# Kernel tuning notes

Hardware: AMD Instinct MI355X
Metric: run time of the kernel (lower is better)

The kernel has to match this reference:

```python
import jax, jax.numpy as jnp
import numpy as np

N = 50000      # nodes
E = 800000     # edges (avg degree 16)
F0 = 3         # node feature dim
EF = 3         # edge feature dim
C = 4          # num classes


def _lin_params(k, din, dout):
    k1, k2 = jax.random.split(k)
    s = 1.0 / np.sqrt(din)
    W = jax.random.uniform(k1, (dout, din), jnp.float32, -s, s)
    b = jax.random.uniform(k2, (dout,), jnp.float32, -s, s)
    return W, b


def setup_inputs() -> dict:
    key = jax.random.key(0)
    ks = jax.random.split(key, 8)
    x = jax.random.normal(ks[0], (N, F0), jnp.float32)
    edge_index = jax.random.randint(ks[1], (2, E), 0, N, jnp.int32)
    edge_attr = jax.random.uniform(ks[2], (E, EF), dtype=jnp.float32)
    W1, b1 = _lin_params(ks[3], 2 * F0 + EF, 128)
    W2, b2 = _lin_params(ks[4], 2 * 128 + EF, 64)
    W3, b3 = _lin_params(ks[5], 2 * 64 + EF, 32)
    Wc, bc = _lin_params(ks[6], 32, C)
    return dict(x=x, edge_index=edge_index, edge_attr=edge_attr,
                W1=W1, b1=b1, W2=W2, b2=b2, W3=W3, b3=b3, Wc=Wc, bc=bc)


def _edgeconv(x, src, dst, ea, W, b, n):
    # message = Linear(cat([x_i, x_j, edge_attr])); aggregated by scatter-add to dst (x_i side).
    # Split W so the node-side matmuls happen once per node instead of per edge.
    f = x.shape[1]
    Wi, Wj, We = W[:, :f], W[:, f:2 * f], W[:, 2 * f:]
    ai = x @ Wi.T   # [N, out]
    aj = x @ Wj.T   # [N, out]
    msg = ai[dst] + aj[src] + ea @ We.T + b  # [E_aug, out]
    return jax.ops.segment_sum(msg, dst, num_segments=n)


def reference(x, edge_index, edge_attr, W1, b1, W2, b2, W3, b3, Wc, bc):
    n = x.shape[0]
    loops = jnp.arange(n, dtype=edge_index.dtype)
    src = jnp.concatenate([edge_index[0], loops])  # x_j indices
    dst = jnp.concatenate([edge_index[1], loops])  # x_i indices (aggregation targets)
    ea = jnp.concatenate([edge_attr, jnp.zeros((n, edge_attr.shape[1]), edge_attr.dtype)])
    h = jax.nn.relu(_edgeconv(x, src, dst, ea, W1, b1, n))
    h = jax.nn.relu(_edgeconv(h, src, dst, ea, W2, b2, n))
    h = _edgeconv(h, src, dst, ea, W3, b3, n)  # no relu after conv3 in the original
    logits = h @ Wc.T + bc
    return jax.nn.log_softmax(logits, axis=1)
```

## Files before the change

### kernel.cpp

```cpp
#include <hip/hip_runtime.h>
#include <math.h>


static inline size_t align256(size_t x) { return (x + 255) & ~size_t(255); }

typedef unsigned short ushort_t;
using frag8  = __attribute__((ext_vector_type(8))) short;
using f32x4v = __attribute__((ext_vector_type(4))) float;
using half8  = __attribute__((ext_vector_type(8))) _Float16;

__device__ inline unsigned short f2bf(float f) {
    unsigned u = __float_as_uint(f);
    unsigned r = (u + 0x7fffu + ((u >> 16) & 1u)) >> 16;
    return (unsigned short)r;
}
__device__ inline float bflo(unsigned u) { return __uint_as_float(u << 16); }
__device__ inline float bfhi(unsigned u) { return __uint_as_float(u & 0xffff0000u); }


__global__ __launch_bounds__(256) void build_count(
    const int* __restrict__ ei, int* __restrict__ count,
    int* __restrict__ pos, int E)
{
    int e4 = (blockIdx.x * 256 + threadIdx.x) * 4;
    if (e4 >= E) return;
    if (e4 + 3 < E) {
        int4 d = *(const int4*)(ei + E + e4);
        int4 po;
        po.x = atomicAdd(&count[d.x], 1);
        po.y = atomicAdd(&count[d.y], 1);
        po.z = atomicAdd(&count[d.z], 1);
        po.w = atomicAdd(&count[d.w], 1);
        *(int4*)(pos + e4) = po;
    } else {
        for (int e = e4; e < E; ++e)
            pos[e] = atomicAdd(&count[ei[E + e]], 1);
    }
}

__global__ __launch_bounds__(256) void scan_pass1(
    const int* __restrict__ count, int* __restrict__ rowstart,
    int* __restrict__ bsum, int n)
{
    __shared__ int sh[256];
    const int tid = threadIdx.x;
    const int base = blockIdx.x * 1024 + tid * 4;
    int v0 = 0, v1 = 0, v2 = 0, v3 = 0;
    if (base + 3 < n) {
        int4 c = *(const int4*)(count + base);
        v0 = c.x; v1 = c.y; v2 = c.z; v3 = c.w;
    } else {
        if (base + 0 < n) v0 = count[base + 0];
        if (base + 1 < n) v1 = count[base + 1];
        if (base + 2 < n) v2 = count[base + 2];
        if (base + 3 < n) v3 = count[base + 3];
    }
    int tsum = v0 + v1 + v2 + v3;
    sh[tid] = tsum;
    __syncthreads();
    for (int off = 1; off < 256; off <<= 1) {
        int t = (tid >= off) ? sh[tid - off] : 0;
        __syncthreads();
        sh[tid] += t;
        __syncthreads();
    }
    int excl = sh[tid] - tsum;
    int p0 = excl + v0, p1 = p0 + v1, p2 = p1 + v2, p3 = p2 + v3;
    if (base + 0 < n) rowstart[base + 1] = p0;
    if (base + 1 < n) rowstart[base + 2] = p1;
    if (base + 2 < n) rowstart[base + 3] = p2;
    if (base + 3 < n) rowstart[base + 4] = p3;
    if (tid == 255) bsum[blockIdx.x] = sh[255];
}

__global__ __launch_bounds__(64) void scan_pass2(
    const int* __restrict__ bsum, int* __restrict__ bexcl, int nb)
{
    int lane = threadIdx.x;
    int own = (lane < nb) ? bsum[lane] : 0;
    int x = own;
    for (int off = 1; off < 64; off <<= 1) {
        int t = __shfl_up(x, off);
        if (lane >= off) x += t;
    }
    bexcl[lane] = x - own;
}

__global__ __launch_bounds__(256) void scan_pass3(
    int* __restrict__ rowstart, const int* __restrict__ bexcl,
    const float* __restrict__ x, float4* __restrict__ xpad, int n)
{
    int j = blockIdx.x * 256 + threadIdx.x;
    if (j > n) return;
    if (j == 0) {
        rowstart[0] = 0;
    } else {
        int b = (j - 1) >> 10;
        if (b > 0) rowstart[j] += bexcl[b];
    }
    if (j < n)
        xpad[j] = make_float4(x[j * 3], x[j * 3 + 1], x[j * 3 + 2], 0.f);
}

__global__ __launch_bounds__(256) void csr_scatter(
    const int* __restrict__ ei, const float* __restrict__ ea,
    const int* __restrict__ pos, const int* __restrict__ rowstart,
    uint2* __restrict__ csrp, int E)
{
    int e4 = (blockIdx.x * 256 + threadIdx.x) * 4;
    if (e4 >= E) return;
    if (e4 + 3 < E) {
        int4 s = *(const int4*)(ei + e4);
        int4 d = *(const int4*)(ei + E + e4);
        int4 po = *(const int4*)(pos + e4);
        float4 a = *(const float4*)(ea + (size_t)e4 * 3);
        float4 b = *(const float4*)(ea + (size_t)e4 * 3 + 4);
        float4 c = *(const float4*)(ea + (size_t)e4 * 3 + 8);
        float ev[12] = { a.x, a.y, a.z, a.w, b.x, b.y, b.z, b.w, c.x, c.y, c.z, c.w };
        int sv[4] = { s.x, s.y, s.z, s.w };
        int dv[4] = { d.x, d.y, d.z, d.w };
        int pv[4] = { po.x, po.y, po.z, po.w };
        #pragma unroll
        for (int r = 0; r < 4; ++r) {
            uint2 p;
            p.x = (unsigned)f2bf(ev[r * 3 + 0]) | ((unsigned)f2bf(ev[r * 3 + 1]) << 16);
            p.y = (unsigned)f2bf(ev[r * 3 + 2]) | ((unsigned)sv[r] << 16);
            csrp[rowstart[dv[r]] + pv[r]] = p;
        }
    } else {
        for (int e = e4; e < E; ++e) {
            uint2 p;
            p.x = (unsigned)f2bf(ea[e * 3 + 0]) | ((unsigned)f2bf(ea[e * 3 + 1]) << 16);
            p.y = (unsigned)f2bf(ea[e * 3 + 2]) | ((unsigned)ei[e] << 16);
            csrp[rowstart[ei[E + e]] + pos[e]] = p;
        }
    }
}


__global__ __launch_bounds__(256) void prep_collapse(
    const float* __restrict__ W3, const float* __restrict__ b3,
    const float* __restrict__ Wc, const float* __restrict__ bc,
    float* __restrict__ AB, float* __restrict__ consts)
{
    int t = threadIdx.x;
    for (int idx = t; idx < 512; idx += 256) {
        int j = idx >> 6, k = idx & 63;
        int jj = j & 3;
        int base = (j >= 4) ? 64 : 0;
        float s = 0.f;
        #pragma unroll
        for (int c = 0; c < 32; ++c)
            s += Wc[jj * 32 + c] * W3[c * 131 + base + k];
        AB[idx] = s;
    }
    if (t < 4) {
        float db = 0.f;
        for (int c = 0; c < 32; ++c) db += Wc[t * 32 + c] * b3[c];
        consts[t] = db;
        consts[4 + t] = bc[t];
        for (int q = 0; q < 3; ++q) {
            float s = 0.f;
            for (int c = 0; c < 32; ++c) s += Wc[t * 32 + c] * W3[c * 131 + 128 + q];
            consts[8 + t * 3 + q] = s;
        }
    }
}


__global__ __launch_bounds__(256) void h1_fused(
    const float4* __restrict__ xpad, const float* __restrict__ W1,
    const float* __restrict__ b1, const int* __restrict__ rowstart,
    const uint2* __restrict__ csrp, float4* __restrict__ eagg4,
    ushort_t* __restrict__ h1, int n_nodes)
{
    __shared__ float sM[10 * 128];
    const int tid = threadIdx.x;
    for (int t = tid; t < 1280; t += 256) {
        int k = t >> 7, c = t & 127;
        sM[t] = (k < 9) ? W1[c * 9 + k] : b1[c];
    }
    __syncthreads();

    int wl = tid & 63;
    int grp = wl >> 3, ch8 = wl & 7;
    int n = blockIdx.x * 32 + (tid >> 6) * 8 + grp;
    if (n >= n_nodes) return;

    int s0 = rowstart[n], s1 = rowstart[n + 1];
    float xx = 0.f, xy = 0.f, xz = 0.f, ex = 0.f, ey = 0.f, ez = 0.f;
    for (int i = s0 + ch8; i < s1; i += 8) {
        uint2 p = csrp[i];
        int s = (int)(p.y >> 16);
        ex += bflo(p.x); ey += bfhi(p.x); ez += bflo(p.y);
        float4 xv = xpad[s];
        xx += xv.x; xy += xv.y; xz += xv.z;
    }
    #pragma unroll
    for (int off = 1; off < 8; off <<= 1) {
        xx += __shfl_xor(xx, off); xy += __shfl_xor(xy, off); xz += __shfl_xor(xz, off);
        ex += __shfl_xor(ex, off); ey += __shfl_xor(ey, off); ez += __shfl_xor(ez, off);
    }

    float deg = (float)(s1 - s0 + 1);
    float4 xs = xpad[n];
    float v[10] = { deg * xs.x, deg * xs.y, deg * xs.z,
                    xs.x + xx, xs.y + xy, xs.z + xz,
                    ex, ey, ez, deg };
    int cb = ch8 * 16;
    #pragma unroll
    for (int g = 0; g < 2; ++g) {
        float hv[8];
        #pragma unroll
        for (int q = 0; q < 8; ++q) {
            int c = cb + g * 8 + q;
            float h = 0.f;
            #pragma unroll
            for (int k = 0; k < 10; ++k) h += v[k] * sM[k * 128 + c];
            hv[q] = fmaxf(h, 0.f);
        }
        uint4 u;
        u.x = (unsigned)f2bf(hv[0]) | ((unsigned)f2bf(hv[1]) << 16);
        u.y = (unsigned)f2bf(hv[2]) | ((unsigned)f2bf(hv[3]) << 16);
        u.z = (unsigned)f2bf(hv[4]) | ((unsigned)f2bf(hv[5]) << 16);
        u.w = (unsigned)f2bf(hv[6]) | ((unsigned)f2bf(hv[7]) << 16);
        *(uint4*)(h1 + (size_t)n * 128 + cb + g * 8) = u;
    }
    if (ch8 == 0) eagg4[n] = make_float4(ex, ey, ez, 0.f);
}


__global__ __launch_bounds__(256) void gemm_mfma(
    const ushort_t* __restrict__ h1, const float* __restrict__ W2,
    float* __restrict__ AI2, _Float16* __restrict__ AJ2, int n_nodes)
{
    constexpr int KP = 136;
    __shared__ ushort_t sB[128 * KP];

    const int tid = threadIdx.x;
    for (int t = tid; t < 128 * 128; t += 256) {
        int jg = t >> 7, k = t & 127;
        float w = (jg < 64) ? W2[jg * 259 + k] : W2[(jg - 64) * 259 + 128 + k];
        sB[jg * KP + k] = f2bf(w);
    }
    __syncthreads();

    const int wave = tid >> 6, lane = tid & 63;
    const int m = lane & 15, quad = lane >> 4;
    const int mwave = blockIdx.x * 64 + wave * 16;

    int arow = mwave + m;
    int arow_c = arow < n_nodes ? arow : (n_nodes - 1);

    frag8 a[4];
    #pragma unroll
    for (int ks = 0; ks < 4; ++ks)
        a[ks] = *(const frag8*)(h1 + (size_t)arow_c * 128 + ks * 32 + quad * 8);

    f32x4v acc[8];
    #pragma unroll
    for (int t = 0; t < 8; ++t) acc[t] = (f32x4v)(0.f);

    #pragma unroll
    for (int t = 0; t < 8; ++t) {
        #pragma unroll
        for (int ks = 0; ks < 4; ++ks) {
            frag8 b = *(const frag8*)(sB + (t * 16 + m) * KP + ks * 32 + quad * 8);
            acc[t] = __builtin_amdgcn_mfma_f32_16x16x32_bf16(a[ks], b, acc[t], 0, 0, 0);
        }
    }

    #pragma unroll
    for (int reg = 0; reg < 4; ++reg) {
        int grow = mwave + quad * 4 + reg;
        if (grow >= n_nodes) continue;
        #pragma unroll
        for (int t = 0; t < 4; ++t)
            AI2[(size_t)grow * 64 + t * 16 + m] = acc[t][reg];
        #pragma unroll
        for (int t = 4; t < 8; ++t)
            AJ2[(size_t)grow * 64 + (t - 4) * 16 + m] = (_Float16)acc[t][reg];
    }
}


__global__ __launch_bounds__(256) void gather2(
    const float* __restrict__ AI2, const _Float16* __restrict__ AJ2,
    const float* __restrict__ W2, const float* __restrict__ b2,
    const float4* __restrict__ eagg4, const int* __restrict__ rowstart,
    const uint2* __restrict__ csrp, const float* __restrict__ AB,
    float* __restrict__ U, float* __restrict__ Z, int n_nodes)
{
    __shared__ float sAB[512];
    __shared__ float sWe[192];
    const int tid = threadIdx.x;
    for (int t = tid; t < 512; t += 256) sAB[t] = AB[t];
    for (int t = tid; t < 192; t += 256) {
        int c = t / 3, q = t % 3;
        sWe[t] = W2[c * 259 + 256 + q];
    }
    __syncthreads();

    int wl = tid & 63;
    int grp = wl >> 3, ch8 = wl & 7;
    int n = blockIdx.x * 32 + (tid >> 6) * 8 + grp;
    if (n >= n_nodes) return;

    int s0 = rowstart[n], s1 = rowstart[n + 1];

    half8 hacc = (half8)(_Float16)0.f;
    for (int base = s0; base < s1; base += 8) {
        int j = base + ch8;
        if (j >= s1) j = s1 - 1;
        int myidx = (int)(csrp[j].y >> 16);
        int cnt = s1 - base; if (cnt > 8) cnt = 8;
        #pragma unroll
        for (int k = 0; k < 8; ++k) {
            int s = __shfl(myidx, grp * 8 + k);
            if (k < cnt) {
                half8 v = *(const half8*)(AJ2 + (size_t)s * 64 + ch8 * 8);
                hacc += v;
            }
        }
    }
    float acc[8];
    #pragma unroll
    for (int q = 0; q < 8; ++q) acc[q] = (float)hacc[q];

    float deg = (float)(s1 - s0 + 1);
    float4 e4 = eagg4[n];
    const float* aip = AI2 + (size_t)n * 64 + ch8 * 8;
    float4 aiA = *(const float4*)(aip);
    float4 aiB = *(const float4*)(aip + 4);
    half8 su = *(const half8*)(AJ2 + (size_t)n * 64 + ch8 * 8);
    float4 bA = *(const float4*)(b2 + ch8 * 8);
    float4 bB = *(const float4*)(b2 + ch8 * 8 + 4);
    float av[8] = { aiA.x, aiA.y, aiA.z, aiA.w, aiB.x, aiB.y, aiB.z, aiB.w };
    float bv[8] = { bA.x, bA.y, bA.z, bA.w, bB.x, bB.y, bB.z, bB.w };
    float r[8];
    #pragma unroll
    for (int q = 0; q < 8; ++q) {
        int c = ch8 * 8 + q;
        float we = sWe[c * 3] * e4.x + sWe[c * 3 + 1] * e4.y + sWe[c * 3 + 2] * e4.z;
        r[q] = fmaxf(deg * (av[q] + bv[q]) + (float)su[q] + we + acc[q], 0.f);
    }
    float pj[8];
    #pragma unroll
    for (int j = 0; j < 8; ++j) {
        float4 wA = *(const float4*)(sAB + j * 64 + ch8 * 8);
        float4 wB = *(const float4*)(sAB + j * 64 + ch8 * 8 + 4);
        pj[j] = r[0] * wA.x + r[1] * wA.y + r[2] * wA.z + r[3] * wA.w
              + r[4] * wB.x + r[5] * wB.y + r[6] * wB.z + r[7] * wB.w;
    }
    #pragma unroll
    for (int off = 1; off < 8; off <<= 1)
        #pragma unroll
        for (int j = 0; j < 8; ++j) pj[j] += __shfl_xor(pj[j], off);

    if (ch8 == 0) {
        *(float4*)(U + (size_t)n * 4) = make_float4(pj[0], pj[1], pj[2], pj[3]);
        *(float4*)(Z + (size_t)n * 4) = make_float4(pj[4], pj[5], pj[6], pj[7]);
    }
}


__global__ __launch_bounds__(256) void final_softmax(
    const float* __restrict__ U, const float* __restrict__ Z,
    const float4* __restrict__ eagg4, const int* __restrict__ rowstart,
    const uint2* __restrict__ csrp, const float* __restrict__ consts,
    float* __restrict__ out, int n_nodes)
{
    int wl = threadIdx.x & 63;
    int grp = wl >> 3, ch8 = wl & 7;
    int n = blockIdx.x * 32 + (threadIdx.x >> 6) * 8 + grp;
    if (n >= n_nodes) return;

    int s0 = rowstart[n], s1 = rowstart[n + 1];
    float ax = 0.f, ay = 0.f, az = 0.f, aw = 0.f;
    for (int i = s0 + ch8; i < s1; i += 8) {
        int s = (int)(csrp[i].y >> 16);
        float4 z = *(const float4*)(Z + (size_t)s * 4);
        ax += z.x; ay += z.y; az += z.z; aw += z.w;
    }
    #pragma unroll
    for (int off = 1; off < 8; off <<= 1) {
        ax += __shfl_xor(ax, off); ay += __shfl_xor(ay, off);
        az += __shfl_xor(az, off); aw += __shfl_xor(aw, off);
    }
    if (ch8 != 0) return;

    float deg = (float)(s1 - s0 + 1);
    float4 u = *(const float4*)(U + (size_t)n * 4);
    float4 zs = *(const float4*)(Z + (size_t)n * 4);
    float4 e4 = eagg4[n];
    float av[4] = { ax + zs.x, ay + zs.y, az + zs.z, aw + zs.w };
    float uv[4] = { u.x, u.y, u.z, u.w };
    float lg[4];
    #pragma unroll
    for (int j = 0; j < 4; ++j) {
        lg[j] = deg * (uv[j] + consts[j]) + av[j] + consts[4 + j]
              + consts[8 + j * 3] * e4.x + consts[9 + j * 3] * e4.y
              + consts[10 + j * 3] * e4.z;
    }
    float m = fmaxf(fmaxf(lg[0], lg[1]), fmaxf(lg[2], lg[3]));
    float lse = logf(expf(lg[0] - m) + expf(lg[1] - m) + expf(lg[2] - m) + expf(lg[3] - m));
    *(float4*)(out + (size_t)n * 4) =
        make_float4(lg[0] - m - lse, lg[1] - m - lse, lg[2] - m - lse, lg[3] - m - lse);
}


extern "C" void kernel_launch(void* const* d_in, const int* in_sizes, int n_in,
                              void* d_out, int out_size, void* d_ws, size_t ws_size,
                              hipStream_t stream)
{
    const float* x    = (const float*)d_in[0];
    const int*   ei   = (const int*)  d_in[1];
    const float* ea   = (const float*)d_in[2];
    const float* W1   = (const float*)d_in[3];
    const float* b1   = (const float*)d_in[4];
    const float* W2   = (const float*)d_in[5];
    const float* b2   = (const float*)d_in[6];
    const float* W3   = (const float*)d_in[7];
    const float* b3   = (const float*)d_in[8];
    const float* Wc   = (const float*)d_in[9];
    const float* bc   = (const float*)d_in[10];
    float* out = (float*)d_out;

    const int N = in_sizes[0] / 3;
    const int E = in_sizes[1] / 2;

    char* ws = (char*)d_ws;
    size_t off = 0;
    int*    count    = (int*)(ws + off);            off = align256(off + (size_t)N * 4);
    int*    pos      = (int*)(ws + off);            off = align256(off + (size_t)E * 4);
    int*    rowstart = (int*)(ws + off);            off = align256(off + (size_t)(N + 1) * 4);
    uint2*  csrp     = (uint2*)(ws + off);          off = align256(off + (size_t)E * 8);
    int*    bsum     = (int*)(ws + off);            off = align256(off + 256);
    int*    bexcl    = (int*)(ws + off);            off = align256(off + 256);
    float*  AB       = (float*)(ws + off);          off = align256(off + 512 * 4);
    float*  consts   = (float*)(ws + off);          off = align256(off + 32 * 4);
    float4* xpad     = (float4*)(ws + off);         off = align256(off + (size_t)N * 16);
    float4* eagg4    = (float4*)(ws + off);         off = align256(off + (size_t)N * 16);
    ushort_t* h1buf  = (ushort_t*)(ws + off);       off = align256(off + (size_t)N * 128 * 2);
    float*  AI2      = (float*)(ws + off);          off = align256(off + (size_t)N * 64 * 4);
    _Float16* AJ2    = (_Float16*)(ws + off);       off = align256(off + (size_t)N * 64 * 2);
    float*  Ubuf     = (float*)(ws + off);          off = align256(off + (size_t)N * 16);
    float*  Zbuf     = (float*)(ws + off);          off = align256(off + (size_t)N * 16);
    (void)ws_size;

    hipMemsetAsync(count, 0, (size_t)N * 4, stream);

    const int eb4 = ((E + 3) / 4 + 255) / 256;
    build_count<<<eb4, 256, 0, stream>>>(ei, count, pos, E);

    const int nb1 = (N + 1023) / 1024;
    scan_pass1<<<nb1, 256, 0, stream>>>(count, rowstart, bsum, N);
    scan_pass2<<<1, 64, 0, stream>>>(bsum, bexcl, nb1);
    scan_pass3<<<(N + 1 + 255) / 256, 256, 0, stream>>>(rowstart, bexcl, x, xpad, N);
    csr_scatter<<<eb4, 256, 0, stream>>>(ei, ea, pos, rowstart, csrp, E);

    prep_collapse<<<1, 256, 0, stream>>>(W3, b3, Wc, bc, AB, consts);

    const int gb = (N + 31) / 32;

    h1_fused<<<gb, 256, 0, stream>>>(xpad, W1, b1, rowstart, csrp, eagg4, h1buf, N);

    gemm_mfma<<<(N + 63) / 64, 256, 0, stream>>>(h1buf, W2, AI2, AJ2, N);
    gather2<<<gb, 256, 0, stream>>>(AI2, AJ2, W2, b2, eagg4, rowstart, csrp, AB, Ubuf, Zbuf, N);

    final_softmax<<<gb, 256, 0, stream>>>(Ubuf, Zbuf, eagg4, rowstart, csrp, consts, out, N);
}
```

Before: 209.4 us.

## Fuse layer-1 aggregation with MFMA GEMM via shared memory; merge small prep kernels

```diff
diff --git a/kernel.cpp b/kernel.cpp
--- a/kernel.cpp
+++ b/kernel.cpp
@@ -73,17 +73,55 @@
     if (tid == 255) bsum[blockIdx.x] = sh[255];
 }
 
-__global__ __launch_bounds__(64) void scan_pass2(
-    const int* __restrict__ bsum, int* __restrict__ bexcl, int nb)
-{
-    int lane = threadIdx.x;
-    int own = (lane < nb) ? bsum[lane] : 0;
-    int x = own;
-    for (int off = 1; off < 64; off <<= 1) {
-        int t = __shfl_up(x, off);
-        if (lane >= off) x += t;
-    }
-    bexcl[lane] = x - own;
+__global__ __launch_bounds__(256) void mid_fused(
+    const int* __restrict__ bsum, int* __restrict__ bexcl, int nb,
+    const float* __restrict__ W3, const float* __restrict__ b3,
+    const float* __restrict__ Wc, const float* __restrict__ bc,
+    float* __restrict__ AB, float* __restrict__ consts,
+    const float* __restrict__ W2, ushort_t* __restrict__ W2bf)
+{
+    const int t = threadIdx.x;
+    if (blockIdx.x == 0) {
+        if (t < 64) {
+            int own = (t < nb) ? bsum[t] : 0;
+            int x = own;
+            for (int off = 1; off < 64; off <<= 1) {
+                int s = __shfl_up(x, off);
+                if (t >= off) x += s;
+            }
+            bexcl[t] = x - own;
+        }
+    } else if (blockIdx.x == 1) {
+        for (int idx = t; idx < 512; idx += 256) {
+            int j = idx >> 6, k = idx & 63;
+            int jj = j & 3;
+            int base = (j >= 4) ? 64 : 0;
+            float s = 0.f;
+            #pragma unroll
+            for (int c = 0; c < 32; ++c)
+                s += Wc[jj * 32 + c] * W3[c * 131 + base + k];
+            AB[idx] = s;
+        }
+        if (t < 4) {
+            float db = 0.f;
+            for (int c = 0; c < 32; ++c) db += Wc[t * 32 + c] * b3[c];
+            consts[t] = db;
+            consts[4 + t] = bc[t];
+            for (int q = 0; q < 3; ++q) {
+                float s = 0.f;
+                for (int c = 0; c < 32; ++c) s += Wc[t * 32 + c] * W3[c * 131 + 128 + q];
+                consts[8 + t * 3 + q] = s;
+            }
+        }
+    } else {
+        int i0 = (blockIdx.x - 2) * 4096 + t;
+        int i1 = (blockIdx.x - 1) * 4096;
+        for (int idx = i0; idx < i1; idx += 256) {
+            int jg = idx >> 7, k = idx & 127;
+            float w = (jg < 64) ? W2[jg * 259 + k] : W2[(jg - 64) * 259 + 128 + k];
+            W2bf[idx] = f2bf(w);
+        }
+    }
 }
 
 __global__ __launch_bounds__(256) void scan_pass3(
@@ -138,43 +176,17 @@
 }
 
 
-__global__ __launch_bounds__(256) void prep_collapse(
-    const float* __restrict__ W3, const float* __restrict__ b3,
-    const float* __restrict__ Wc, const float* __restrict__ bc,
-    float* __restrict__ AB, float* __restrict__ consts)
-{
-    int t = threadIdx.x;
-    for (int idx = t; idx < 512; idx += 256) {
-        int j = idx >> 6, k = idx & 63;
-        int jj = j & 3;
-        int base = (j >= 4) ? 64 : 0;
-        float s = 0.f;
-        #pragma unroll
-        for (int c = 0; c < 32; ++c)
-            s += Wc[jj * 32 + c] * W3[c * 131 + base + k];
-        AB[idx] = s;
-    }
-    if (t < 4) {
-        float db = 0.f;
-        for (int c = 0; c < 32; ++c) db += Wc[t * 32 + c] * b3[c];
-        consts[t] = db;
-        consts[4 + t] = bc[t];
-        for (int q = 0; q < 3; ++q) {
-            float s = 0.f;
-            for (int c = 0; c < 32; ++c) s += Wc[t * 32 + c] * W3[c * 131 + 128 + q];
-            consts[8 + t * 3 + q] = s;
-        }
-    }
-}
-
-
-__global__ __launch_bounds__(256) void h1_fused(
+__global__ __launch_bounds__(256) void h1_gemm(
     const float4* __restrict__ xpad, const float* __restrict__ W1,
     const float* __restrict__ b1, const int* __restrict__ rowstart,
     const uint2* __restrict__ csrp, float4* __restrict__ eagg4,
-    ushort_t* __restrict__ h1, int n_nodes)
-{
+    const ushort_t* __restrict__ W2bf,
+    float* __restrict__ AI2, _Float16* __restrict__ AJ2, int n_nodes)
+{
+    constexpr int HS = 144;
     __shared__ float sM[10 * 128];
+    __shared__ ushort_t sH[64 * HS];
+
     const int tid = threadIdx.x;
     for (int t = tid; t < 1280; t += 256) {
         int k = t >> 7, c = t & 127;
@@ -182,80 +194,66 @@
     }
     __syncthreads();
 
-    int wl = tid & 63;
-    int grp = wl >> 3, ch8 = wl & 7;
-    int n = blockIdx.x * 32 + (tid >> 6) * 8 + grp;
-    if (n >= n_nodes) return;
-
-    int s0 = rowstart[n], s1 = rowstart[n + 1];
-    float xx = 0.f, xy = 0.f, xz = 0.f, ex = 0.f, ey = 0.f, ez = 0.f;
-    for (int i = s0 + ch8; i < s1; i += 8) {
-        uint2 p = csrp[i];
-        int s = (int)(p.y >> 16);
-        ex += bflo(p.x); ey += bfhi(p.x); ez += bflo(p.y);
-        float4 xv = xpad[s];
-        xx += xv.x; xy += xv.y; xz += xv.z;
-    }
-    #pragma unroll
-    for (int off = 1; off < 8; off <<= 1) {
-        xx += __shfl_xor(xx, off); xy += __shfl_xor(xy, off); xz += __shfl_xor(xz, off);
-        ex += __shfl_xor(ex, off); ey += __shfl_xor(ey, off); ez += __shfl_xor(ez, off);
-    }
-
-    float deg = (float)(s1 - s0 + 1);
-    float4 xs = xpad[n];
-    float v[10] = { deg * xs.x, deg * xs.y, deg * xs.z,
-                    xs.x + xx, xs.y + xy, xs.z + xz,
-                    ex, ey, ez, deg };
-    int cb = ch8 * 16;
-    #pragma unroll
-    for (int g = 0; g < 2; ++g) {
-        float hv[8];
-        #pragma unroll
-        for (int q = 0; q < 8; ++q) {
-            int c = cb + g * 8 + q;
-            float h = 0.f;
+    const int base = blockIdx.x * 64;
+    const int wave = tid >> 6, wl = tid & 63;
+    const int grp = wl >> 3, ch8 = wl & 7;
+
+    #pragma unroll
+    for (int pass = 0; pass < 2; ++pass) {
+        int nl = pass * 32 + wave * 8 + grp;
+        int n = base + nl;
+        float hv[16];
+        if (n < n_nodes) {
+            int s0 = rowstart[n], s1 = rowstart[n + 1];
+            float xx = 0.f, xy = 0.f, xz = 0.f, ex = 0.f, ey = 0.f, ez = 0.f;
+            for (int i = s0 + ch8; i < s1; i += 8) {
+                uint2 p = csrp[i];
+                int s = (int)(p.y >> 16);
+                ex += bflo(p.x); ey += bfhi(p.x); ez += bflo(p.y);
+                float4 xv = xpad[s];
+                xx += xv.x; xy += xv.y; xz += xv.z;
+            }
             #pragma unroll
-            for (int k = 0; k < 10; ++k) h += v[k] * sM[k * 128 + c];
-            hv[q] = fmaxf(h, 0.f);
-        }
-        uint4 u;
-        u.x = (unsigned)f2bf(hv[0]) | ((unsigned)f2bf(hv[1]) << 16);
-        u.y = (unsigned)f2bf(hv[2]) | ((unsigned)f2bf(hv[3]) << 16);
-        u.z = (unsigned)f2bf(hv[4]) | ((unsigned)f2bf(hv[5]) << 16);
-        u.w = (unsigned)f2bf(hv[6]) | ((unsigned)f2bf(hv[7]) << 16);
-        *(uint4*)(h1 + (size_t)n * 128 + cb + g * 8) = u;
-    }
-    if (ch8 == 0) eagg4[n] = make_float4(ex, ey, ez, 0.f);
-}
-
-
-__global__ __launch_bounds__(256) void gemm_mfma(
-    const ushort_t* __restrict__ h1, const float* __restrict__ W2,
-    float* __restrict__ AI2, _Float16* __restrict__ AJ2, int n_nodes)
-{
-    constexpr int KP = 136;
-    __shared__ ushort_t sB[128 * KP];
-
-    const int tid = threadIdx.x;
-    for (int t = tid; t < 128 * 128; t += 256) {
-        int jg = t >> 7, k = t & 127;
-        float w = (jg < 64) ? W2[jg * 259 + k] : W2[(jg - 64) * 259 + 128 + k];
-        sB[jg * KP + k] = f2bf(w);
+            for (int off = 1; off < 8; off <<= 1) {
+                xx += __shfl_xor(xx, off); xy += __shfl_xor(xy, off); xz += __shfl_xor(xz, off);
+                ex += __shfl_xor(ex, off); ey += __shfl_xor(ey, off); ez += __shfl_xor(ez, off);
+            }
+            float deg = (float)(s1 - s0 + 1);
+            float4 xs = xpad[n];
+            float v[10] = { deg * xs.x, deg * xs.y, deg * xs.z,
+                            xs.x + xx, xs.y + xy, xs.z + xz,
+                            ex, ey, ez, deg };
+            #pragma unroll
+            for (int q = 0; q < 16; ++q) {
+                int c = ch8 * 16 + q;
+                float h = 0.f;
+                #pragma unroll
+                for (int k = 0; k < 10; ++k) h += v[k] * sM[k * 128 + c];
+                hv[q] = fmaxf(h, 0.f);
+            }
+            if (ch8 == 0) eagg4[n] = make_float4(ex, ey, ez, 0.f);
+        } else {
+            #pragma unroll
+            for (int q = 0; q < 16; ++q) hv[q] = 0.f;
+        }
+        #pragma unroll
+        for (int g = 0; g < 2; ++g) {
+            uint4 u;
+            u.x = (unsigned)f2bf(hv[g * 8 + 0]) | ((unsigned)f2bf(hv[g * 8 + 1]) << 16);
+            u.y = (unsigned)f2bf(hv[g * 8 + 2]) | ((unsigned)f2bf(hv[g * 8 + 3]) << 16);
+            u.z = (unsigned)f2bf(hv[g * 8 + 4]) | ((unsigned)f2bf(hv[g * 8 + 5]) << 16);
+            u.w = (unsigned)f2bf(hv[g * 8 + 6]) | ((unsigned)f2bf(hv[g * 8 + 7]) << 16);
+            *(uint4*)(sH + nl * HS + ch8 * 16 + g * 8) = u;
+        }
     }
     __syncthreads();
 
-    const int wave = tid >> 6, lane = tid & 63;
-    const int m = lane & 15, quad = lane >> 4;
-    const int mwave = blockIdx.x * 64 + wave * 16;
-
-    int arow = mwave + m;
-    int arow_c = arow < n_nodes ? arow : (n_nodes - 1);
+    const int m = wl & 15, quad = wl >> 4;
 
     frag8 a[4];
     #pragma unroll
     for (int ks = 0; ks < 4; ++ks)
-        a[ks] = *(const frag8*)(h1 + (size_t)arow_c * 128 + ks * 32 + quad * 8);
+        a[ks] = *(const frag8*)(sH + (wave * 16 + m) * HS + ks * 32 + quad * 8);
 
     f32x4v acc[8];
     #pragma unroll
@@ -265,14 +263,14 @@
     for (int t = 0; t < 8; ++t) {
         #pragma unroll
         for (int ks = 0; ks < 4; ++ks) {
-            frag8 b = *(const frag8*)(sB + (t * 16 + m) * KP + ks * 32 + quad * 8);
+            frag8 b = *(const frag8*)(W2bf + (t * 16 + m) * 128 + ks * 32 + quad * 8);
             acc[t] = __builtin_amdgcn_mfma_f32_16x16x32_bf16(a[ks], b, acc[t], 0, 0, 0);
         }
     }
 
     #pragma unroll
     for (int reg = 0; reg < 4; ++reg) {
-        int grow = mwave + quad * 4 + reg;
+        int grow = base + wave * 16 + quad * 4 + reg;
         if (grow >= n_nodes) continue;
         #pragma unroll
         for (int t = 0; t < 4; ++t)
@@ -308,7 +306,8 @@
 
     int s0 = rowstart[n], s1 = rowstart[n + 1];
 
-    half8 hacc = (half8)(_Float16)0.f;
+    half8 hacc0 = (half8)(_Float16)0.f;
+    half8 hacc1 = (half8)(_Float16)0.f;
     for (int base = s0; base < s1; base += 8) {
         int j = base + ch8;
         if (j >= s1) j = s1 - 1;
@@ -319,13 +318,13 @@
             int s = __shfl(myidx, grp * 8 + k);
             if (k < cnt) {
                 half8 v = *(const half8*)(AJ2 + (size_t)s * 64 + ch8 * 8);
-                hacc += v;
+                if (k & 1) hacc1 += v; else hacc0 += v;
             }
         }
     }
     float acc[8];
     #pragma unroll
-    for (int q = 0; q < 8; ++q) acc[q] = (float)hacc[q];
+    for (int q = 0; q < 8; ++q) acc[q] = (float)hacc0[q] + (float)hacc1[q];
 
     float deg = (float)(s1 - s0 + 1);
     float4 e4 = eagg4[n];
@@ -439,9 +438,9 @@
     int*    bexcl    = (int*)(ws + off);            off = align256(off + 256);
     float*  AB       = (float*)(ws + off);          off = align256(off + 512 * 4);
     float*  consts   = (float*)(ws + off);          off = align256(off + 32 * 4);
+    ushort_t* W2bf   = (ushort_t*)(ws + off);       off = align256(off + 128 * 128 * 2);
     float4* xpad     = (float4*)(ws + off);         off = align256(off + (size_t)N * 16);
     float4* eagg4    = (float4*)(ws + off);         off = align256(off + (size_t)N * 16);
-    ushort_t* h1buf  = (ushort_t*)(ws + off);       off = align256(off + (size_t)N * 128 * 2);
     float*  AI2      = (float*)(ws + off);          off = align256(off + (size_t)N * 64 * 4);
     _Float16* AJ2    = (_Float16*)(ws + off);       off = align256(off + (size_t)N * 64 * 2);
     float*  Ubuf     = (float*)(ws + off);          off = align256(off + (size_t)N * 16);
@@ -455,17 +454,14 @@
 
     const int nb1 = (N + 1023) / 1024;
     scan_pass1<<<nb1, 256, 0, stream>>>(count, rowstart, bsum, N);
-    scan_pass2<<<1, 64, 0, stream>>>(bsum, bexcl, nb1);
+    mid_fused<<<6, 256, 0, stream>>>(bsum, bexcl, nb1, W3, b3, Wc, bc, AB, consts, W2, W2bf);
     scan_pass3<<<(N + 1 + 255) / 256, 256, 0, stream>>>(rowstart, bexcl, x, xpad, N);
     csr_scatter<<<eb4, 256, 0, stream>>>(ei, ea, pos, rowstart, csrp, E);
 
-    prep_collapse<<<1, 256, 0, stream>>>(W3, b3, Wc, bc, AB, consts);
+    h1_gemm<<<(N + 63) / 64, 256, 0, stream>>>(xpad, W1, b1, rowstart, csrp,
+                                               eagg4, W2bf, AI2, AJ2, N);
 
     const int gb = (N + 31) / 32;
-
-    h1_fused<<<gb, 256, 0, stream>>>(xpad, W1, b1, rowstart, csrp, eagg4, h1buf, N);
-
-    gemm_mfma<<<(N + 63) / 64, 256, 0, stream>>>(h1buf, W2, AI2, AJ2, N);
     gather2<<<gb, 256, 0, stream>>>(AI2, AJ2, W2, b2, eagg4, rowstart, csrp, AB, Ubuf, Zbuf, N);
 
     final_softmax<<<gb, 256, 0, stream>>>(Ubuf, Zbuf, eagg4, rowstart, csrp, consts, out, N);
```

Measured after the change: 203.0 us (median of 2 runs). 1.03x faster.
